# Optimization experiments

Measured on AMD Instinct MI355X. Metric: run time of the kernel, lower is better.

Reference implementation:

```python
import jax, jax.numpy as jnp
import numpy as np
from jax import lax

B, C, H, W = 16, 1, 1024, 1024
BOUNDARY_WEIGHT = 3.0
# two iterations of a flat 5x5 structuring element == one flat 9x9 window
WIN = 9
PAD = WIN // 2


def setup_inputs() -> dict:
    key = jax.random.key(0)
    k1, k2, k3, k4 = jax.random.split(key, 4)
    logits = jax.random.normal(k1, (B, C, H, W), dtype=jnp.float32)
    # spatially-coherent binary masks (random disks), mimicking car masks
    cy = jax.random.uniform(k2, (B,), minval=0.3 * H, maxval=0.7 * H)
    cx = jax.random.uniform(k3, (B,), minval=0.3 * W, maxval=0.7 * W)
    r = jax.random.uniform(k4, (B,), minval=0.15 * H, maxval=0.4 * H)
    ys = jnp.arange(H, dtype=jnp.float32)
    xs = jnp.arange(W, dtype=jnp.float32)
    d2 = (ys[None, :, None] - cy[:, None, None]) ** 2 + (xs[None, None, :] - cx[:, None, None]) ** 2
    targets = (d2 < (r[:, None, None] ** 2)).astype(jnp.float32)[:, None]  # [B,1,H,W]
    return {"logits": logits, "targets": targets}


def _morph(t, op, init):
    # flat-SE morphology over HxW via reduce_window; cv2 default border is
    # the neutral value for the op, matching init padding.
    return lax.reduce_window(
        t, init, op,
        window_dimensions=(1, 1, WIN, WIN),
        window_strides=(1, 1, 1, 1),
        padding=[(0, 0), (0, 0), (PAD, PAD), (PAD, PAD)],
    )


def reference(logits, targets):
    dilated = _morph(targets, lax.max, -jnp.inf)
    eroded = _morph(targets, lax.min, jnp.inf)
    boundary = dilated - eroded  # 1 on mask boundary band, else 0
    weights = 1.0 + (BOUNDARY_WEIGHT - 1.0) * boundary
    # stable BCE-with-logits: max(x,0) - x*y + log1p(exp(-|x|))
    x, y = logits, targets
    per_elem = jnp.maximum(x, 0.0) - x * y + jax.nn.softplus(-jnp.abs(x))
    return jnp.mean(weights * per_elem)
```

## Files before the change

kernel.cpp:

```cpp
#include <hip/hip_runtime.h>

#define BATCH 16
#define IMG_H 1024
#define IMG_W 1024
#define WORDS 16
typedef unsigned long long u64;

__global__ void wbce_zero_kernel(float* out) { out[0] = 0.0f; }

#define PK_NT 256
#define PK_BLOCKS 2048
__global__ __launch_bounds__(PK_NT, 8)
void wbce_pack_kernel(const float* __restrict__ tgt, u64* __restrict__ pak)
{
    const int lane = threadIdx.x & 63;
    const int gw   = blockIdx.x * (PK_NT / 64) + (threadIdx.x >> 6);
    #pragma unroll
    for (int i = 0; i < 8; ++i) {
        int g = gw + i * (PK_BLOCKS * (PK_NT / 64));
        const float* p = tgt + (size_t)g * 256 + lane;
        float v0 = p[0], v1 = p[64], v2 = p[128], v3 = p[192];
        u64 m0 = __ballot(v0 > 0.5f);
        u64 m1 = __ballot(v1 > 0.5f);
        u64 m2 = __ballot(v2 > 0.5f);
        u64 m3 = __ballot(v3 > 0.5f);
        if (lane == 0) {
            ulonglong2* q = (ulonglong2*)(pak + (size_t)g * 4);
            q[0] = make_ulonglong2(m0, m1);
            q[1] = make_ulonglong2(m2, m3);
        }
    }
}

#define BC_NT 512
#define TY 16
#define SR (TY + 8)
#define NWAVES (BC_NT / 64)

__global__ __launch_bounds__(BC_NT, 8)
void wbce_bce_kernel(const float* __restrict__ logits,
                     const u64* __restrict__ pak,
                     float* __restrict__ out)
{
    __shared__ u64 sPak[SR * WORDS];
    __shared__ u64 sHD [SR * WORDS];
    __shared__ u64 sHE [SR * WORDS];
    __shared__ u64 sBnd[TY * WORDS];
    __shared__ float sRed[NWAVES];

    const int tid  = threadIdx.x;
    const int lane = tid & 63;
    const int wv   = tid >> 6;
    const int rowBase = blockIdx.x * TY;
    const int b = blockIdx.y;

    const u64*  pb = pak    + (size_t)b * (IMG_H * WORDS);
    const float* lg = logits + (size_t)b * (IMG_H * IMG_W);

    if (tid < SR * WORDS) {
        int sr = tid >> 4, w = tid & 15;
        int gr = rowBase + sr - 4;
        u64 hd = 0ULL, he = ~0ULL, C = 0ULL;
        if (gr >= 0 && gr < IMG_H) {
            const u64* rp = pb + (size_t)gr * WORDS;
            C = rp[w];
            u64 P  = (w > 0)  ? rp[w - 1] : 0ULL;
            u64 N  = (w < 15) ? rp[w + 1] : 0ULL;
            u64 Pe = (w > 0)  ? P : ~0ULL;
            u64 Ne = (w < 15) ? N : ~0ULL;
            u64 d = C, e = C;
            #pragma unroll
            for (int s = 1; s <= 4; ++s) {
                d |= (C >> s) | (N  << (64 - s));
                d |= (C << s) | (P  >> (64 - s));
                e &= (C >> s) | (Ne << (64 - s));
                e &= (C << s) | (Pe >> (64 - s));
            }
            hd = d; he = e;
        }
        sPak[tid] = C;
        sHD[tid]  = hd;
        sHE[tid]  = he;
    }
    __syncthreads();

    if (tid < TY * WORDS) {
        int r = tid >> 4, w = tid & 15;
        u64 d = 0ULL, e = ~0ULL;
        #pragma unroll
        for (int k = 0; k < 9; ++k) {
            d |= sHD[(r + k) * WORDS + w];
            e &= sHE[(r + k) * WORDS + w];
        }
        sBnd[tid] = d & ~e;
    }
    __syncthreads();

    float acc = 0.0f;
    #pragma unroll
    for (int k = 0; k < (TY * IMG_W / 4) / BC_NT; ++k) {
        int it  = tid + k * BC_NT;
        int r   = it >> 8;
        int pos = it & 255;
        int w   = pos >> 4;
        int sh  = (pos & 15) * 4;

        float4 x4 = *(const float4*)(lg + (size_t)(rowBase + r) * IMG_W + pos * 4);
        unsigned int bb = (unsigned int)(sBnd[r * WORDS + w] >> sh);
        unsigned int tb = (unsigned int)(sPak[(r + 4) * WORDS + w] >> sh);

        const float xs[4] = {x4.x, x4.y, x4.z, x4.w};
        #pragma unroll
        for (int j = 0; j < 4; ++j) {
            float x  = xs[j];
            float wg = 1.0f + 2.0f * (float)((bb >> j) & 1u);
            float y  = (float)((tb >> j) & 1u);
            float a  = fabsf(x);
            float t  = __builtin_exp2f(a * -1.44269504088896340736f);
            float sp = __builtin_log2f(1.0f + t) * 0.69314718055994530942f;
            float pe = fmaxf(x, 0.0f) - x * y + sp;
            acc = fmaf(wg, pe, acc);
        }
    }

    #pragma unroll
    for (int off = 32; off > 0; off >>= 1)
        acc += __shfl_down(acc, off, 64);
    if (lane == 0) sRed[wv] = acc;
    __syncthreads();
    if (tid == 0) {
        float s = 0.0f;
        #pragma unroll
        for (int i = 0; i < NWAVES; ++i) s += sRed[i];
        atomicAdd(out, s * (1.0f / 16777216.0f));
    }
}

extern "C" void kernel_launch(void* const* d_in, const int* in_sizes, int n_in,
                              void* d_out, int out_size, void* d_ws, size_t ws_size,
                              hipStream_t stream) {
    const float* logits  = (const float*)d_in[0];
    const float* targets = (const float*)d_in[1];
    float* out = (float*)d_out;
    u64* pak = (u64*)d_ws;

    wbce_zero_kernel<<<dim3(1), dim3(1), 0, stream>>>(out);

    wbce_pack_kernel<<<dim3(PK_BLOCKS), dim3(PK_NT), 0, stream>>>(targets, pak);

    dim3 grid(IMG_H / TY, BATCH);
    wbce_bce_kernel<<<grid, dim3(BC_NT), 0, stream>>>(logits, pak, out);
}
```

Measured before the change: 42.14 us.

## Split morphology into separate kernel and stream BCE over flat grid-stride layout

Moves the 9x9 bitwise dilation/erosion out of the BCE kernel into its own kernel, which writes interleaved target/boundary 32-bit words. The BCE kernel becomes a flat grid-stride loop with no shared-memory staging or block syncs. It also folds the zeroing of the output into the pack kernel, removing one launch, and simplifies the per-element math with sign-flip bit tricks. The cost is one extra kernel launch and a round trip of the boundary bitmap through global memory.

```diff
diff --git a/kernel.cpp b/kernel.cpp
--- a/kernel.cpp
+++ b/kernel.cpp
@@ -4,20 +4,25 @@
 #define IMG_H 1024
 #define IMG_W 1024
 #define WORDS 16
+#define TOTAL_WORDS (BATCH * IMG_H * WORDS)
 typedef unsigned long long u64;
-
-__global__ void wbce_zero_kernel(float* out) { out[0] = 0.0f; }
 
 #define PK_NT 256
 #define PK_BLOCKS 2048
+#define PK_WAVES (PK_NT / 64)
+#define GROUPS (TOTAL_WORDS / 4)
+#define PK_ITERS (GROUPS / (PK_BLOCKS * PK_WAVES))
+
 __global__ __launch_bounds__(PK_NT, 8)
-void wbce_pack_kernel(const float* __restrict__ tgt, u64* __restrict__ pak)
+void wbce_pack_kernel(const float* __restrict__ tgt, u64* __restrict__ pak,
+                      float* __restrict__ out)
 {
+    if (blockIdx.x == 0 && threadIdx.x == 0) out[0] = 0.0f;
     const int lane = threadIdx.x & 63;
-    const int gw   = blockIdx.x * (PK_NT / 64) + (threadIdx.x >> 6);
+    const int gw   = blockIdx.x * PK_WAVES + (threadIdx.x >> 6);
     #pragma unroll
-    for (int i = 0; i < 8; ++i) {
-        int g = gw + i * (PK_BLOCKS * (PK_NT / 64));
+    for (int i = 0; i < PK_ITERS; ++i) {
+        int g = gw + i * (PK_BLOCKS * PK_WAVES);
         const float* p = tgt + (size_t)g * 256 + lane;
         float v0 = p[0], v1 = p[64], v2 = p[128], v3 = p[192];
         u64 m0 = __ballot(v0 > 0.5f);
@@ -32,93 +37,80 @@
     }
 }
 
-#define BC_NT 512
-#define TY 16
-#define SR (TY + 8)
-#define NWAVES (BC_NT / 64)
+#define MO_NT 256
+__global__ __launch_bounds__(MO_NT, 8)
+void wbce_morph_kernel(const u64* __restrict__ pak, uint4* __restrict__ tbnd)
+{
+    const int idx = blockIdx.x * MO_NT + threadIdx.x;
+    const int w   = idx & 15;
+    const int row = (idx >> 4) & (IMG_H - 1);
+    const int img = idx >> 14;
+    const u64* ib = pak + (size_t)img * (IMG_H * WORDS);
 
-__global__ __launch_bounds__(BC_NT, 8)
+    u64 d = 0ULL, e = ~0ULL, C = 0ULL;
+    const int r0 = row >= 4 ? row - 4 : 0;
+    const int r1 = row <= IMG_H - 5 ? row + 4 : IMG_H - 1;
+    for (int r = r0; r <= r1; ++r) {
+        const u64* rp = ib + (size_t)r * WORDS;
+        u64 c  = rp[w];
+        u64 P  = (w > 0)  ? rp[w - 1] : 0ULL;
+        u64 N  = (w < 15) ? rp[w + 1] : 0ULL;
+        u64 Pe = (w > 0)  ? P : ~0ULL;
+        u64 Ne = (w < 15) ? N : ~0ULL;
+        u64 hd = c, he = c;
+        #pragma unroll
+        for (int s = 1; s <= 4; ++s) {
+            hd |= (c >> s) | (N  << (64 - s));
+            hd |= (c << s) | (P  >> (64 - s));
+            he &= (c >> s) | (Ne << (64 - s));
+            he &= (c << s) | (Pe >> (64 - s));
+        }
+        d |= hd;
+        e &= he;
+        if (r == row) C = c;
+    }
+    u64 bnd = d & ~e;
+    tbnd[idx] = make_uint4((unsigned)C,          (unsigned)bnd,
+                           (unsigned)(C >> 32),  (unsigned)(bnd >> 32));
+}
+
+#define BC_NT 256
+#define BC_BLOCKS 2048
+#define TOTAL_F4 (BATCH * IMG_H * IMG_W / 4)
+#define BC_STRIDE (BC_NT * BC_BLOCKS)
+#define BC_ITERS (TOTAL_F4 / BC_STRIDE)
+#define BC_NWAVES (BC_NT / 64)
+
+__global__ __launch_bounds__(BC_NT, 6)
 void wbce_bce_kernel(const float* __restrict__ logits,
-                     const u64* __restrict__ pak,
+                     const uint2* __restrict__ tbnd,
                      float* __restrict__ out)
 {
-    __shared__ u64 sPak[SR * WORDS];
-    __shared__ u64 sHD [SR * WORDS];
-    __shared__ u64 sHE [SR * WORDS];
-    __shared__ u64 sBnd[TY * WORDS];
-    __shared__ float sRed[NWAVES];
-
-    const int tid  = threadIdx.x;
-    const int lane = tid & 63;
-    const int wv   = tid >> 6;
-    const int rowBase = blockIdx.x * TY;
-    const int b = blockIdx.y;
-
-    const u64*  pb = pak    + (size_t)b * (IMG_H * WORDS);
-    const float* lg = logits + (size_t)b * (IMG_H * IMG_W);
-
-    if (tid < SR * WORDS) {
-        int sr = tid >> 4, w = tid & 15;
-        int gr = rowBase + sr - 4;
-        u64 hd = 0ULL, he = ~0ULL, C = 0ULL;
-        if (gr >= 0 && gr < IMG_H) {
-            const u64* rp = pb + (size_t)gr * WORDS;
-            C = rp[w];
-            u64 P  = (w > 0)  ? rp[w - 1] : 0ULL;
-            u64 N  = (w < 15) ? rp[w + 1] : 0ULL;
-            u64 Pe = (w > 0)  ? P : ~0ULL;
-            u64 Ne = (w < 15) ? N : ~0ULL;
-            u64 d = C, e = C;
-            #pragma unroll
-            for (int s = 1; s <= 4; ++s) {
-                d |= (C >> s) | (N  << (64 - s));
-                d |= (C << s) | (P  >> (64 - s));
-                e &= (C >> s) | (Ne << (64 - s));
-                e &= (C << s) | (Pe >> (64 - s));
-            }
-            hd = d; he = e;
-        }
-        sPak[tid] = C;
-        sHD[tid]  = hd;
-        sHE[tid]  = he;
-    }
-    __syncthreads();
-
-    if (tid < TY * WORDS) {
-        int r = tid >> 4, w = tid & 15;
-        u64 d = 0ULL, e = ~0ULL;
-        #pragma unroll
-        for (int k = 0; k < 9; ++k) {
-            d |= sHD[(r + k) * WORDS + w];
-            e &= sHE[(r + k) * WORDS + w];
-        }
-        sBnd[tid] = d & ~e;
-    }
-    __syncthreads();
+    __shared__ float sRed[BC_NWAVES];
+    const int tid = threadIdx.x;
+    const int i0  = blockIdx.x * BC_NT + tid;
+    const float4* lg4 = (const float4*)logits;
 
     float acc = 0.0f;
     #pragma unroll
-    for (int k = 0; k < (TY * IMG_W / 4) / BC_NT; ++k) {
-        int it  = tid + k * BC_NT;
-        int r   = it >> 8;
-        int pos = it & 255;
-        int w   = pos >> 4;
-        int sh  = (pos & 15) * 4;
-
-        float4 x4 = *(const float4*)(lg + (size_t)(rowBase + r) * IMG_W + pos * 4);
-        unsigned int bb = (unsigned int)(sBnd[r * WORDS + w] >> sh);
-        unsigned int tb = (unsigned int)(sPak[(r + 4) * WORDS + w] >> sh);
+    for (int k = 0; k < BC_ITERS; ++k) {
+        int it = i0 + k * BC_STRIDE;
+        float4 x4 = lg4[it];
+        uint2  tb = tbnd[it >> 3];
+        int    sh = (it & 7) * 4;
 
         const float xs[4] = {x4.x, x4.y, x4.z, x4.w};
         #pragma unroll
         for (int j = 0; j < 4; ++j) {
-            float x  = xs[j];
-            float wg = 1.0f + 2.0f * (float)((bb >> j) & 1u);
-            float y  = (float)((tb >> j) & 1u);
-            float a  = fabsf(x);
-            float t  = __builtin_exp2f(a * -1.44269504088896340736f);
-            float sp = __builtin_log2f(1.0f + t) * 0.69314718055994530942f;
-            float pe = fmaxf(x, 0.0f) - x * y + sp;
+            unsigned tbit = (tb.x >> (sh + j)) & 1u;
+            unsigned bbit = (tb.y >> (sh + j)) & 1u;
+            unsigned xu   = __float_as_uint(xs[j]);
+            float sgn = __uint_as_float(xu ^ (tbit << 31));
+            float a   = __uint_as_float(xu & 0x7fffffffu);
+            float t   = __builtin_exp2f(a * -1.44269504088896340736f);
+            float l2  = __builtin_log2f(1.0f + t);
+            float pe  = fmaf(l2, 0.69314718055994530942f, fmaxf(sgn, 0.0f));
+            float wg  = fmaf((float)bbit, 2.0f, 1.0f);
             acc = fmaf(wg, pe, acc);
         }
     }
@@ -126,12 +118,13 @@
     #pragma unroll
     for (int off = 32; off > 0; off >>= 1)
         acc += __shfl_down(acc, off, 64);
+    const int lane = tid & 63, wv = tid >> 6;
     if (lane == 0) sRed[wv] = acc;
     __syncthreads();
     if (tid == 0) {
         float s = 0.0f;
         #pragma unroll
-        for (int i = 0; i < NWAVES; ++i) s += sRed[i];
+        for (int i = 0; i < BC_NWAVES; ++i) s += sRed[i];
         atomicAdd(out, s * (1.0f / 16777216.0f));
     }
 }
@@ -142,12 +135,14 @@
     const float* logits  = (const float*)d_in[0];
     const float* targets = (const float*)d_in[1];
     float* out = (float*)d_out;
-    u64* pak = (u64*)d_ws;
 
-    wbce_zero_kernel<<<dim3(1), dim3(1), 0, stream>>>(out);
+    u64*   pak  = (u64*)d_ws;
+    uint4* tbnd = (uint4*)(pak + TOTAL_WORDS);
 
-    wbce_pack_kernel<<<dim3(PK_BLOCKS), dim3(PK_NT), 0, stream>>>(targets, pak);
+    wbce_pack_kernel<<<dim3(PK_BLOCKS), dim3(PK_NT), 0, stream>>>(targets, pak, out);
 
-    dim3 grid(IMG_H / TY, BATCH);
-    wbce_bce_kernel<<<grid, dim3(BC_NT), 0, stream>>>(logits, pak, out);
+    wbce_morph_kernel<<<dim3(TOTAL_WORDS / MO_NT), dim3(MO_NT), 0, stream>>>(pak, tbnd);
+
+    wbce_bce_kernel<<<dim3(BC_BLOCKS), dim3(BC_NT), 0, stream>>>(
+        logits, (const uint2*)tbnd, out);
 }
```

Measured after the change: 60.02 us. 1.42x slower.
